# Kernel tuning notes

Measured on AMD Instinct MI355X. Metric: run time of the kernel, lower is better.

## Reference

```python
import jax, jax.numpy as jnp
import numpy as np

B, T, L = 64, 128, 32          # batch, read timesteps, item_len (write phase)
D, R = 256, 1024               # output_dim (= input dim per step), controller rnn_size
N, M = 512, 128                # memory_rows, memory_columns
RH, WH = 1, 1                  # read / write heads
EPS = 1e-8
SCALE = 0.02


def setup_inputs() -> dict:
    key = jax.random.key(0)
    ks = jax.random.split(key, 6)
    in_dim = D + RH * M                      # controller sees [x_t, prev reads]
    head_dim = RH * (M + 6) + WH * (3 * M + 6)  # k,beta,g,s(3),gamma (+erase,add for write)
    return {
        "inputs": jax.random.normal(ks[0], (B, T, D), jnp.float32),
        "W_lstm": jax.random.normal(ks[1], (in_dim, 4 * R), jnp.float32) * SCALE,
        "U_lstm": jax.random.normal(ks[2], (R, 4 * R), jnp.float32) * SCALE,
        "b_lstm": jnp.zeros((4 * R,), jnp.float32),
        "W_heads": jax.random.normal(ks[3], (R, head_dim), jnp.float32) * SCALE,
        "b_heads": jnp.zeros((head_dim,), jnp.float32),
        "W_out": jax.random.normal(ks[4], (R + RH * M, D), jnp.float32) * SCALE,
        "b_out": jnp.zeros((D,), jnp.float32),
    }


def _address(Mem, Mem_norm, k, beta, g, s, gamma, w_prev):
    """NTM content + location addressing. Mem:[B,N,M], returns w:[B,N]."""
    k = jnp.tanh(k)                                   # [B,M]
    beta = jax.nn.softplus(beta)                      # [B,1]
    g = jax.nn.sigmoid(g)                             # [B,1]
    s = jax.nn.softmax(s, axis=-1)                    # [B,3] shifts (-1,0,1)
    gamma = 1.0 + jax.nn.softplus(gamma)              # [B,1]
    # cosine similarity content addressing
    sim = jnp.einsum('bnm,bm->bn', Mem, k) / (
        Mem_norm * jnp.linalg.norm(k, axis=-1, keepdims=True) + EPS)
    w_c = jax.nn.softmax(beta * sim, axis=-1)
    # interpolate with previous weighting
    w_g = g * w_c + (1.0 - g) * w_prev
    # circular convolutional shift over {-1,0,1}
    w_s = (s[:, 0:1] * jnp.roll(w_g, -1, axis=-1)
           + s[:, 1:2] * w_g
           + s[:, 2:3] * jnp.roll(w_g, 1, axis=-1))
    # sharpen
    w_pow = (w_s + EPS) ** gamma
    return w_pow / jnp.sum(w_pow, axis=-1, keepdims=True)


def _run(inputs, W_lstm, U_lstm, b_lstm, W_heads, b_heads, W_out, b_out):
    def step(carry, x_t):
        h, c, reads, w_r, w_w, Mem = carry
        # LSTM controller
        z = jnp.concatenate([x_t, reads], -1) @ W_lstm + h @ U_lstm + b_lstm
        zi, zf, zg, zo = jnp.split(z, 4, axis=-1)
        c = jax.nn.sigmoid(zf) * c + jax.nn.sigmoid(zi) * jnp.tanh(zg)
        h = jax.nn.sigmoid(zo) * jnp.tanh(c)
        # head parameters
        p = h @ W_heads + b_heads
        Mem_norm = jnp.linalg.norm(Mem, axis=-1)  # [B,N]
        new_w_r, new_reads = [], []
        for hh in range(RH):
            o = hh * (M + 6)
            w = _address(Mem, Mem_norm, p[:, o:o + M], p[:, o + M:o + M + 1],
                         p[:, o + M + 1:o + M + 2], p[:, o + M + 2:o + M + 5],
                         p[:, o + M + 5:o + M + 6], w_r[:, hh])
            new_w_r.append(w)
            new_reads.append(jnp.einsum('bn,bnm->bm', w, Mem))
        base, wsz = RH * (M + 6), 3 * M + 6
        new_w_w = []
        for hh in range(WH):
            o = base + hh * wsz
            w = _address(Mem, Mem_norm, p[:, o:o + M], p[:, o + M:o + M + 1],
                         p[:, o + M + 1:o + M + 2], p[:, o + M + 2:o + M + 5],
                         p[:, o + M + 5:o + M + 6], w_w[:, hh])
            erase = jax.nn.sigmoid(p[:, o + M + 6:o + 2 * M + 6])
            add = jnp.tanh(p[:, o + 2 * M + 6:o + 3 * M + 6])
            Mem = Mem * (1.0 - w[:, :, None] * erase[:, None, :]) + w[:, :, None] * add[:, None, :]
            new_w_w.append(w)
        reads = jnp.concatenate(new_reads, -1)
        out = jnp.concatenate([h, reads], -1) @ W_out + b_out
        carry = (h, c, reads, jnp.stack(new_w_r, 1), jnp.stack(new_w_w, 1), Mem)
        return carry, out

    init = (jnp.zeros((B, R)), jnp.zeros((B, R)), jnp.zeros((B, RH * M)),
            jnp.full((B, RH, N), 1.0 / N), jnp.full((B, WH, N), 1.0 / N),
            jnp.full((B, N, M), 1e-6))
    # read phase (inputs) followed by write phase (zero response sheet)
    xs = jnp.concatenate([inputs, jnp.zeros((B, L, D), inputs.dtype)], axis=1)
    xs = jnp.moveaxis(xs, 0, 1)  # [T+L, B, D]
    _, outs = jax.lax.scan(step, init, xs)
    write_outputs = jax.nn.sigmoid(jnp.moveaxis(outs[T:], 0, 1))  # [B, L, D]
    return write_outputs


def reference(inputs, W_lstm, U_lstm, b_lstm, W_heads, b_heads, W_out, b_out):
    return _run(inputs, W_lstm, U_lstm, b_lstm, W_heads, b_heads, W_out, b_out)
```

## Files before the change

kernel.cpp:

```cpp
#include <hip/hip_runtime.h>
#include <hip/hip_fp16.h>
#include <math.h>

#define B 64
#define T_READ 128
#define L_WRITE 32
#define TT 160
#define D 256
#define R 1024
#define N 512
#define M 128
#define HD 524
#define K5K 1152
#define EPS 1e-8f
#define BNM ((size_t)B*N*M)

__device__ __forceinline__ float sigmoidf(float x){ return 1.0f/(1.0f+expf(-x)); }
__device__ __forceinline__ float softplusf(float x){ return (x > 20.f) ? x : log1pf(expf(x)); }

__global__ __launch_bounds__(256) void kx_transpose(const float* __restrict__ x, float* __restrict__ xT){
    __shared__ float tile[64][65];
    const int t = blockIdx.x >> 2, k0 = (blockIdx.x & 3)*64;
    #pragma unroll
    for (int rep = 0; rep < 16; ++rep){
        int idx = rep*256 + threadIdx.x;
        int bl = idx >> 6, kl = idx & 63;
        tile[bl][kl] = x[((size_t)bl*T_READ + t)*D + k0 + kl];
    }
    __syncthreads();
    #pragma unroll
    for (int rep = 0; rep < 16; ++rep){
        int idx = rep*256 + threadIdx.x;
        int kl = idx >> 6, bl = idx & 63;
        xT[((size_t)t*D + k0 + kl)*64 + bl] = tile[bl][kl];
    }
}

__global__ __launch_bounds__(256) void kpack_w(const float* __restrict__ Wl, const float* __restrict__ Ul,
                                               __half* __restrict__ Wreh){
    const int k = blockIdx.x;
    const float* src = (k < 384) ? (Wl + (size_t)k*4096) : (Ul + (size_t)(k-384)*4096);
    #pragma unroll
    for (int it = 0; it < 16; ++it){
        int j = it*256 + threadIdx.x;
        int bk = j >> 4, r = j & 15, q = r >> 2, i = r & 3;
        Wreh[((size_t)bk*1408 + k)*16 + r] = __float2half_rn(src[q*1024 + bk*4 + i]);
    }
}

__global__ __launch_bounds__(256) void kpack_wh(const float* __restrict__ Wh, __half* __restrict__ Whh){
    const int k = blockIdx.x;
    for (int j = threadIdx.x; j < HD; j += 256)
        Whh[(size_t)k*HD + j] = __float2half_rn(Wh[(size_t)k*HD + j]);
}

__global__ void k_init(float* ht, float* c_t, float* rp, float* wst, __half* Mem){
    size_t idx = (size_t)blockIdx.x*blockDim.x + threadIdx.x;
    size_t stride = (size_t)gridDim.x*blockDim.x;
    const __half mi = __float2half(1e-6f);
    for (size_t i = idx; i < BNM; i += stride) Mem[i] = mi;
    for (size_t i = idx; i < R*64; i += stride){ ht[i]=0.f; c_t[i]=0.f; }
    for (size_t i = idx; i < 8*128*64; i += stride) rp[i] = 0.f;
    for (size_t i = idx; i < 4*B*N; i += stride) wst[i] = 1.f/512.f;
}

__global__ __launch_bounds__(1024) void k1_z(
    const float* __restrict__ xT, const __half* __restrict__ Wreh, const float* __restrict__ bl,
    float* __restrict__ ht, float* __restrict__ c_t, const float* __restrict__ rp,
    float* __restrict__ hist, int t)
{
    __shared__ float smem[8192 + 16384];
    const int bk = blockIdx.x;
    const int tid = threadIdx.x, lane = tid & 63, w = tid >> 6;

    for (int e = tid; e < 8192; e += 1024){
        float s = 0.f;
        #pragma unroll
        for (int p = 0; p < 8; ++p) s += rp[p*8192 + e];
        smem[e] = s;
        if (t > T_READ && (e >> 10) == bk)
            hist[((size_t)(t-1-T_READ)*K5K + 1024 + (e>>6))*64 + (e&63)] = s;
    }
    __syncthreads();

    const int r0 = bk*4;
    const int rd = (t < T_READ);
    const int kn = rd ? 88 : 72;
    const int k0 = rd ? w*88 : 256 + w*72;
    const __half* wbase = Wreh + ((size_t)bk*1408 + k0)*16;
    float acc[16];
    #pragma unroll
    for (int i = 0; i < 16; ++i) acc[i] = 0.f;
    #pragma unroll 4
    for (int kk = 0; kk < kn; ++kk){
        int k = k0 + kk;
        float a;
        if (k < 256)      a = xT[((size_t)t*256 + k)*64 + lane];
        else if (k < 384) a = smem[(k-256)*64 + lane];
        else              a = ht[(size_t)(k-384)*64 + lane];
        float4 raw0 = *reinterpret_cast<const float4*>(wbase + (size_t)kk*16);
        float4 raw1 = *reinterpret_cast<const float4*>(wbase + (size_t)kk*16 + 8);
        const __half2* h0 = reinterpret_cast<const __half2*>(&raw0);
        const __half2* h1 = reinterpret_cast<const __half2*>(&raw1);
        float2 f;
        f = __half22float2(h0[0]); acc[0] += a*f.x; acc[1] += a*f.y;
        f = __half22float2(h0[1]); acc[2] += a*f.x; acc[3] += a*f.y;
        f = __half22float2(h0[2]); acc[4] += a*f.x; acc[5] += a*f.y;
        f = __half22float2(h0[3]); acc[6] += a*f.x; acc[7] += a*f.y;
        f = __half22float2(h1[0]); acc[8] += a*f.x; acc[9] += a*f.y;
        f = __half22float2(h1[1]); acc[10]+= a*f.x; acc[11]+= a*f.y;
        f = __half22float2(h1[2]); acc[12]+= a*f.x; acc[13]+= a*f.y;
        f = __half22float2(h1[3]); acc[14]+= a*f.x; acc[15]+= a*f.y;
    }
    float* comb = smem + 8192;
    #pragma unroll
    for (int j = 0; j < 16; ++j) comb[(w*16 + j)*64 + lane] = acc[j];
    __syncthreads();
    if (tid < 256){
        int i = tid >> 6, b2 = tid & 63;
        float g4[4];
        #pragma unroll
        for (int q = 0; q < 4; ++q){
            float s = bl[q*1024 + r0 + i];
            #pragma unroll
            for (int ks = 0; ks < 16; ++ks) s += comb[(ks*16 + q*4 + i)*64 + b2];
            g4[q] = s;
        }
        int ri = (r0 + i)*64 + b2;
        float cn = sigmoidf(g4[1])*c_t[ri] + sigmoidf(g4[0])*tanhf(g4[2]);
        float hn = sigmoidf(g4[3])*tanhf(cn);
        c_t[ri] = cn;
        ht[ri] = hn;
        if (t >= T_READ) hist[((size_t)(t-T_READ)*K5K + r0 + i)*64 + b2] = hn;
    }
}

__global__ __launch_bounds__(512) void k2f(
    const float* __restrict__ ht, const __half* __restrict__ Whh, const float* __restrict__ bh,
    float* __restrict__ khat, float* __restrict__ scal, float* __restrict__ eal)
{
    __shared__ float part[8][2][64];
    const int tid = threadIdx.x, lane = tid & 63, w = tid >> 6;
    const int col0 = blockIdx.x*2;
    const int k0 = w*128;
    float a0 = 0.f, a1 = 0.f;
    #pragma unroll 4
    for (int k = k0; k < k0+128; ++k){
        float a = ht[(size_t)k*64 + lane];
        __half2 wv = *reinterpret_cast<const __half2*>(Whh + (size_t)k*HD + col0);
        float2 f = __half22float2(wv);
        a0 += a*f.x; a1 += a*f.y;
    }
    part[w][0][lane] = a0;
    part[w][1][lane] = a1;
    __syncthreads();
    if (tid < 128){
        int c = tid >> 6, b = tid & 63;
        int col = col0 + c;
        float v = bh[col];
        #pragma unroll
        for (int w2 = 0; w2 < 8; ++w2) v += part[w2][c][b];
        if (col < 128)       khat[b*256 + col] = tanhf(v);
        else if (col < 134){ int i = col-128; scal[b*16 + i]     = (i==0)?softplusf(v):(i==1)?sigmoidf(v):(i==5)?1.f+softplusf(v):v; }
        else if (col < 262)  khat[b*256 + 128 + (col-134)] = tanhf(v);
        else if (col < 268){ int i = col-262; scal[b*16 + 8 + i] = (i==0)?softplusf(v):(i==1)?sigmoidf(v):(i==5)?1.f+softplusf(v):v; }
        else if (col < 396)  eal[b*256 + (col-268)]        = sigmoidf(v);
        else                 eal[b*256 + 128 + (col-396)]  = tanhf(v);
    }
}

__global__ __launch_bounds__(512) void k3_dots(
    const float* __restrict__ khat, const __half* __restrict__ Mem,
    float* __restrict__ mnorm, float* __restrict__ dots)
{
    __shared__ float kh[256];
    const int b = blockIdx.x >> 3, nq = blockIdx.x & 7;
    const int tid = threadIdx.x, lane = tid & 63, w = tid >> 6;
    if (tid < 256) kh[tid] = khat[b*256 + tid];
    __syncthreads();
    float2 kr  = reinterpret_cast<const float2*>(kh)[lane];
    float2 kw2 = reinterpret_cast<const float2*>(kh + 128)[lane];
    #pragma unroll 2
    for (int i = 0; i < 8; ++i){
        int n = nq*64 + w*8 + i;
        const __half* mrow = Mem + ((size_t)b*N + n)*M;
        __half2 mh = *reinterpret_cast<const __half2*>(mrow + lane*2);
        float2 mv = __half22float2(mh);
        float s2 = mv.x*mv.x + mv.y*mv.y;
        float dr = mv.x*kr.x + mv.y*kr.y;
        float dw = mv.x*kw2.x + mv.y*kw2.y;
        #pragma unroll
        for (int off = 32; off; off >>= 1){
            s2 += __shfl_xor(s2, off);
            dr += __shfl_xor(dr, off);
            dw += __shfl_xor(dw, off);
        }
        if (lane == 0){
            mnorm[b*N + n] = sqrtf(s2);
            dots[(b*2+0)*N + n] = dr;
            dots[(b*2+1)*N + n] = dw;
        }
    }
}

__device__ __forceinline__ float blk_sum8g(float v, volatile float* red8, int lane, int wgi){
    #pragma unroll
    for (int off = 32; off; off >>= 1) v += __shfl_xor(v, off);
    if (lane == 0) red8[wgi] = v;
    __syncthreads();
    float r = red8[0]+red8[1]+red8[2]+red8[3]+red8[4]+red8[5]+red8[6]+red8[7];
    __syncthreads();
    return r;
}
__device__ __forceinline__ float blk_max8g(float v, volatile float* red8, int lane, int wgi){
    #pragma unroll
    for (int off = 32; off; off >>= 1) v = fmaxf(v, __shfl_xor(v, off));
    if (lane == 0) red8[wgi] = v;
    __syncthreads();
    float r = fmaxf(fmaxf(fmaxf(red8[0],red8[1]),fmaxf(red8[2],red8[3])),
                    fmaxf(fmaxf(red8[4],red8[5]),fmaxf(red8[6],red8[7])));
    __syncthreads();
    return r;
}

__global__ __launch_bounds__(1024) void k4_addr(
    const float* __restrict__ khat, const float* __restrict__ scal, const float* __restrict__ ealg,
    const float* __restrict__ mnorm, const float* __restrict__ dots,
    float* __restrict__ wst, __half* __restrict__ Mem, float* __restrict__ rp, int t)
{
    __shared__ float kh[256];
    __shared__ float sc[16];
    __shared__ float eal[256];
    __shared__ float wfin[1024];
    __shared__ float wgbuf[1024];
    __shared__ float red8[2][8];
    __shared__ float racc_s[1024];
    const int b = blockIdx.x >> 3, nq = blockIdx.x & 7;
    const int tid = threadIdx.x, lane = tid & 63;

    if (tid < 256)      kh[tid]      = khat[b*256 + tid];
    else if (tid < 272) sc[tid-256]  = scal[b*16 + (tid-256)];
    else if (tid < 528) eal[tid-272] = ealg[b*256 + (tid-272)];
    __syncthreads();

    {
        const int g = tid >> 9;
        const int n = tid & 511;
        const int wgi = (tid >> 6) & 7;
        float* wgl = wgbuf + g*512;
        volatile float* r8 = red8[g];

        float kv = (n < 128) ? kh[g*128 + n] : 0.f;
        float knm = sqrtf(blk_sum8g(kv*kv, r8, lane, wgi));
        float beta = sc[g*8+0], gg = sc[g*8+1], gamma = sc[g*8+5];
        float s0r = sc[g*8+2], s1r = sc[g*8+3], s2r = sc[g*8+4];
        float smx = fmaxf(s0r, fmaxf(s1r, s2r));
        float e0 = expf(s0r-smx), e1 = expf(s1r-smx), e2 = expf(s2r-smx);
        float esum = e0+e1+e2;
        float s0 = e0/esum, s1 = e1/esum, s2 = e2/esum;

        float sim = dots[(b*2+g)*N + n] / (mnorm[b*N + n]*knm + EPS);
        float aa = beta * sim;
        float amax = blk_max8g(aa, r8, lane, wgi);
        float ev = expf(aa - amax);
        float wc = ev / blk_sum8g(ev, r8, lane, wgi);

        const float* wpr = wst + ((size_t)((t&1)*2 + g))*(B*N);
        float*       wnx = wst + ((size_t)(((t+1)&1)*2 + g))*(B*N);
        float wprev = wpr[b*N + n];
        float wgv = gg*wc + (1.f - gg)*wprev;
        wgl[n] = wgv; __syncthreads();
        float wsv = s0*wgl[(n+1)&511] + s1*wgv + s2*wgl[(n-1)&511];
        float wp2 = powf(wsv + EPS, gamma);
        float wsum = blk_sum8g(wp2, r8, lane, wgi);
        float wv = wp2 / wsum;
        wfin[g*512 + n] = wv;
        if (nq == 0) wnx[b*N + n] = wv;
        __syncthreads();
    }

    {
        const int m = tid & 127, ns = tid >> 7;
        const float e  = eal[m];
        const float ad = eal[128 + m];
        float racc = 0.f;
        #pragma unroll 4
        for (int i2 = 0; i2 < 8; ++i2){
            int nn = nq*64 + i2*8 + ns;
            size_t idx = ((size_t)b*N + nn)*M + m;
            float v = __half2float(Mem[idx]);
            float wr = wfin[nn], ww = wfin[512 + nn];
            racc += wr*v;
            Mem[idx] = __float2half_rn(v*(1.f - ww*e) + ww*ad);
        }
        racc_s[tid] = racc;
        __syncthreads();
        if (tid < 128){
            float s = 0.f;
            #pragma unroll
            for (int g2 = 0; g2 < 8; ++g2) s += racc_s[g2*128 + tid];
            rp[(size_t)nq*8192 + tid*64 + b] = s;
        }
    }
}

__global__ __launch_bounds__(256) void k_fin(const float* __restrict__ rp, float* __restrict__ hist){
    int e = blockIdx.x*256 + threadIdx.x;
    float s = 0.f;
    #pragma unroll
    for (int p = 0; p < 8; ++p) s += rp[p*8192 + e];
    hist[((size_t)31*K5K + 1024 + (e>>6))*64 + (e&63)] = s;
}

__global__ __launch_bounds__(512) void k5_out(
    const float* __restrict__ hist, const float* __restrict__ Wo, const float* __restrict__ bo,
    float* __restrict__ out)
{
    __shared__ float smem[16384];
    const int tid = threadIdx.x, lane = tid & 63, w = tid >> 6;
    const int l = blockIdx.x >> 3, jg = blockIdx.x & 7;
    const int j0 = jg*32;
    float acc[32];
    #pragma unroll
    for (int i = 0; i < 32; ++i) acc[i] = 0.f;
    const int k0 = w*144;
    #pragma unroll 2
    for (int kk = 0; kk < 144; ++kk){
        int k = k0 + kk;
        float a = hist[((size_t)l*K5K + k)*64 + lane];
        const float* wrow = Wo + (size_t)k*D + j0;
        #pragma unroll
        for (int qq = 0; qq < 8; ++qq){
            float4 wv = *reinterpret_cast<const float4*>(wrow + qq*4);
            acc[qq*4+0] += a*wv.x; acc[qq*4+1] += a*wv.y;
            acc[qq*4+2] += a*wv.z; acc[qq*4+3] += a*wv.w;
        }
    }
    __syncthreads();
    #pragma unroll
    for (int c = 0; c < 32; ++c) smem[(w*32 + c)*64 + lane] = acc[c];
    __syncthreads();
    {
        const int b2 = tid >> 3, jq = tid & 7;
        float4 ov;
        float* po = (float*)&ov;
        #pragma unroll
        for (int i = 0; i < 4; ++i){
            int c = jq*4 + i;
            float s = bo[j0 + c];
            #pragma unroll
            for (int ks = 0; ks < 8; ++ks) s += smem[(ks*32 + c)*64 + b2];
            po[i] = sigmoidf(s);
        }
        *reinterpret_cast<float4*>(out + ((size_t)b2*L_WRITE + l)*D + j0 + jq*4) = ov;
    }
}

extern "C" void kernel_launch(void* const* d_in, const int* in_sizes, int n_in,
                              void* d_out, int out_size, void* d_ws, size_t ws_size,
                              hipStream_t stream)
{
    const float* x   = (const float*)d_in[0];
    const float* Wl  = (const float*)d_in[1];
    const float* Ul  = (const float*)d_in[2];
    const float* bl  = (const float*)d_in[3];
    const float* Wh  = (const float*)d_in[4];
    const float* bh  = (const float*)d_in[5];
    const float* Wo  = (const float*)d_in[6];
    const float* bo  = (const float*)d_in[7];
    float* out = (float*)d_out;

    float* ws = (float*)d_ws;
    float* xT    = ws; ws += (size_t)T_READ*D*64;
    __half* Wreh = (__half*)ws; ws += (size_t)1408*4096/2;
    __half* Whh  = (__half*)ws; ws += (size_t)1024*HD/2 + 64;
    float* ht    = ws; ws += (size_t)R*64;
    float* c_t   = ws; ws += (size_t)R*64;
    float* khat  = ws; ws += (size_t)B*256;
    float* scal  = ws; ws += (size_t)B*16;
    float* eal   = ws; ws += (size_t)B*256;
    float* mnorm = ws; ws += (size_t)B*N;
    float* dots  = ws; ws += (size_t)B*2*N;
    float* wst   = ws; ws += (size_t)4*B*N;
    __half* Mem  = (__half*)ws; ws += BNM/2;
    float* rp    = ws; ws += (size_t)8*128*64;
    float* hist  = ws; ws += (size_t)L_WRITE*K5K*64;

    hipLaunchKernelGGL(kx_transpose, dim3(T_READ*4), dim3(256), 0, stream, x, xT);
    hipLaunchKernelGGL(kpack_w,      dim3(1408),     dim3(256), 0, stream, Wl, Ul, Wreh);
    hipLaunchKernelGGL(kpack_wh,     dim3(1024),     dim3(256), 0, stream, Wh, Whh);
    hipLaunchKernelGGL(k_init,       dim3(2048),     dim3(256), 0, stream, ht, c_t, rp, wst, Mem);

    for (int t = 0; t < TT; ++t){
        hipLaunchKernelGGL(k1_z,    dim3(256), dim3(1024), 0, stream, xT, Wreh, bl, ht, c_t, rp, hist, t);
        hipLaunchKernelGGL(k2f,     dim3(262), dim3(512),  0, stream, ht, Whh, bh, khat, scal, eal);
        hipLaunchKernelGGL(k3_dots, dim3(512), dim3(512),  0, stream, khat, Mem, mnorm, dots);
        hipLaunchKernelGGL(k4_addr, dim3(512), dim3(1024), 0, stream, khat, scal, eal, mnorm, dots, wst, Mem, rp, t);
    }
    hipLaunchKernelGGL(k_fin,  dim3(32),  dim3(256), 0, stream, rp, hist);
    hipLaunchKernelGGL(k5_out, dim3(256), dim3(512), 0, stream, hist, Wo, bo, out);
}
```

Measured before the change: 11.28 ms.

## Replace partial-read buffer reduction with double-buffered atomic accumulation

Per-step read vectors were stored as 8 partial slices, and every k1_z block summed all of them into shared memory. Now k4_addr atomically adds its partials into one of two ping-pong buffers, which k3_dots of the next step zeroes, so k1_z reads the finished vector straight from global memory. This removes the redundant 8-way reduction that all 256 blocks repeated, at the cost of atomic traffic and non-deterministic summation order. Separately, k2f now uses 1024 threads with a 64-row K split per wave instead of 128, to add parallelism to the head projection.

```diff
diff --git a/kernel.cpp b/kernel.cpp
--- a/kernel.cpp
+++ b/kernel.cpp
@@ -54,34 +54,30 @@
         Whh[(size_t)k*HD + j] = __float2half_rn(Wh[(size_t)k*HD + j]);
 }
 
-__global__ void k_init(float* ht, float* c_t, float* rp, float* wst, __half* Mem){
+__global__ void k_init(float* ht, float* c_t, float* reads_fin, float* wst, __half* Mem){
     size_t idx = (size_t)blockIdx.x*blockDim.x + threadIdx.x;
     size_t stride = (size_t)gridDim.x*blockDim.x;
     const __half mi = __float2half(1e-6f);
     for (size_t i = idx; i < BNM; i += stride) Mem[i] = mi;
     for (size_t i = idx; i < R*64; i += stride){ ht[i]=0.f; c_t[i]=0.f; }
-    for (size_t i = idx; i < 8*128*64; i += stride) rp[i] = 0.f;
+    for (size_t i = idx; i < 2*128*64; i += stride) reads_fin[i] = 0.f;
     for (size_t i = idx; i < 4*B*N; i += stride) wst[i] = 1.f/512.f;
 }
 
 __global__ __launch_bounds__(1024) void k1_z(
     const float* __restrict__ xT, const __half* __restrict__ Wreh, const float* __restrict__ bl,
-    float* __restrict__ ht, float* __restrict__ c_t, const float* __restrict__ rp,
+    float* __restrict__ ht, float* __restrict__ c_t, const float* __restrict__ reads_fin,
     float* __restrict__ hist, int t)
 {
-    __shared__ float smem[8192 + 16384];
+    __shared__ float comb[16384];
     const int bk = blockIdx.x;
     const int tid = threadIdx.x, lane = tid & 63, w = tid >> 6;
-
-    for (int e = tid; e < 8192; e += 1024){
-        float s = 0.f;
-        #pragma unroll
-        for (int p = 0; p < 8; ++p) s += rp[p*8192 + e];
-        smem[e] = s;
-        if (t > T_READ && (e >> 10) == bk)
-            hist[((size_t)(t-1-T_READ)*K5K + 1024 + (e>>6))*64 + (e&63)] = s;
-    }
-    __syncthreads();
+    const float* rf = reads_fin + (size_t)(t & 1)*8192;
+
+    if (t > T_READ && bk < 8){
+        int e = bk*1024 + tid;
+        hist[((size_t)(t-1-T_READ)*K5K + 1024 + (e>>6))*64 + (e&63)] = rf[e];
+    }
 
     const int r0 = bk*4;
     const int rd = (t < T_READ);
@@ -96,7 +92,7 @@
         int k = k0 + kk;
         float a;
         if (k < 256)      a = xT[((size_t)t*256 + k)*64 + lane];
-        else if (k < 384) a = smem[(k-256)*64 + lane];
+        else if (k < 384) a = rf[(k-256)*64 + lane];
         else              a = ht[(size_t)(k-384)*64 + lane];
         float4 raw0 = *reinterpret_cast<const float4*>(wbase + (size_t)kk*16);
         float4 raw1 = *reinterpret_cast<const float4*>(wbase + (size_t)kk*16 + 8);
@@ -112,7 +108,6 @@
         f = __half22float2(h1[2]); acc[12]+= a*f.x; acc[13]+= a*f.y;
         f = __half22float2(h1[3]); acc[14]+= a*f.x; acc[15]+= a*f.y;
     }
-    float* comb = smem + 8192;
     #pragma unroll
     for (int j = 0; j < 16; ++j) comb[(w*16 + j)*64 + lane] = acc[j];
     __syncthreads();
@@ -135,17 +130,17 @@
     }
 }
 
-__global__ __launch_bounds__(512) void k2f(
+__global__ __launch_bounds__(1024) void k2f(
     const float* __restrict__ ht, const __half* __restrict__ Whh, const float* __restrict__ bh,
     float* __restrict__ khat, float* __restrict__ scal, float* __restrict__ eal)
 {
-    __shared__ float part[8][2][64];
+    __shared__ float part[16][2][64];
     const int tid = threadIdx.x, lane = tid & 63, w = tid >> 6;
     const int col0 = blockIdx.x*2;
-    const int k0 = w*128;
+    const int k0 = w*64;
     float a0 = 0.f, a1 = 0.f;
     #pragma unroll 4
-    for (int k = k0; k < k0+128; ++k){
+    for (int k = k0; k < k0+64; ++k){
         float a = ht[(size_t)k*64 + lane];
         __half2 wv = *reinterpret_cast<const __half2*>(Whh + (size_t)k*HD + col0);
         float2 f = __half22float2(wv);
@@ -159,7 +154,7 @@
         int col = col0 + c;
         float v = bh[col];
         #pragma unroll
-        for (int w2 = 0; w2 < 8; ++w2) v += part[w2][c][b];
+        for (int w2 = 0; w2 < 16; ++w2) v += part[w2][c][b];
         if (col < 128)       khat[b*256 + col] = tanhf(v);
         else if (col < 134){ int i = col-128; scal[b*16 + i]     = (i==0)?softplusf(v):(i==1)?sigmoidf(v):(i==5)?1.f+softplusf(v):v; }
         else if (col < 262)  khat[b*256 + 128 + (col-134)] = tanhf(v);
@@ -171,11 +166,16 @@
 
 __global__ __launch_bounds__(512) void k3_dots(
     const float* __restrict__ khat, const __half* __restrict__ Mem,
-    float* __restrict__ mnorm, float* __restrict__ dots)
+    float* __restrict__ mnorm, float* __restrict__ dots, float* __restrict__ reads_fin, int t)
 {
     __shared__ float kh[256];
     const int b = blockIdx.x >> 3, nq = blockIdx.x & 7;
     const int tid = threadIdx.x, lane = tid & 63, w = tid >> 6;
+    if (blockIdx.x < 8){
+        int e = blockIdx.x*1024 + tid;
+        reads_fin[(size_t)(t & 1)*8192 + e] = 0.f;
+        reads_fin[(size_t)(t & 1)*8192 + e + 512] = 0.f;
+    }
     if (tid < 256) kh[tid] = khat[b*256 + tid];
     __syncthreads();
     float2 kr  = reinterpret_cast<const float2*>(kh)[lane];
@@ -226,7 +226,7 @@
 __global__ __launch_bounds__(1024) void k4_addr(
     const float* __restrict__ khat, const float* __restrict__ scal, const float* __restrict__ ealg,
     const float* __restrict__ mnorm, const float* __restrict__ dots,
-    float* __restrict__ wst, __half* __restrict__ Mem, float* __restrict__ rp, int t)
+    float* __restrict__ wst, __half* __restrict__ Mem, float* __restrict__ reads_fin, int t)
 {
     __shared__ float kh[256];
     __shared__ float sc[16];
@@ -299,16 +299,14 @@
             float s = 0.f;
             #pragma unroll
             for (int g2 = 0; g2 < 8; ++g2) s += racc_s[g2*128 + tid];
-            rp[(size_t)nq*8192 + tid*64 + b] = s;
-        }
-    }
-}
-
-__global__ __launch_bounds__(256) void k_fin(const float* __restrict__ rp, float* __restrict__ hist){
+            atomicAdd(&reads_fin[(size_t)((t+1) & 1)*8192 + tid*64 + b], s);
+        }
+    }
+}
+
+__global__ __launch_bounds__(256) void k_fin(const float* __restrict__ reads_fin, float* __restrict__ hist){
     int e = blockIdx.x*256 + threadIdx.x;
-    float s = 0.f;
-    #pragma unroll
-    for (int p = 0; p < 8; ++p) s += rp[p*8192 + e];
+    float s = reads_fin[(size_t)(TT & 1)*8192 + e];
     hist[((size_t)31*K5K + 1024 + (e>>6))*64 + (e&63)] = s;
 }
 
@@ -383,20 +381,20 @@
     float* dots  = ws; ws += (size_t)B*2*N;
     float* wst   = ws; ws += (size_t)4*B*N;
     __half* Mem  = (__half*)ws; ws += BNM/2;
-    float* rp    = ws; ws += (size_t)8*128*64;
+    float* reads_fin = ws; ws += (size_t)2*128*64;
     float* hist  = ws; ws += (size_t)L_WRITE*K5K*64;
 
     hipLaunchKernelGGL(kx_transpose, dim3(T_READ*4), dim3(256), 0, stream, x, xT);
     hipLaunchKernelGGL(kpack_w,      dim3(1408),     dim3(256), 0, stream, Wl, Ul, Wreh);
     hipLaunchKernelGGL(kpack_wh,     dim3(1024),     dim3(256), 0, stream, Wh, Whh);
-    hipLaunchKernelGGL(k_init,       dim3(2048),     dim3(256), 0, stream, ht, c_t, rp, wst, Mem);
+    hipLaunchKernelGGL(k_init,       dim3(2048),     dim3(256), 0, stream, ht, c_t, reads_fin, wst, Mem);
 
     for (int t = 0; t < TT; ++t){
-        hipLaunchKernelGGL(k1_z,    dim3(256), dim3(1024), 0, stream, xT, Wreh, bl, ht, c_t, rp, hist, t);
-        hipLaunchKernelGGL(k2f,     dim3(262), dim3(512),  0, stream, ht, Whh, bh, khat, scal, eal);
-        hipLaunchKernelGGL(k3_dots, dim3(512), dim3(512),  0, stream, khat, Mem, mnorm, dots);
-        hipLaunchKernelGGL(k4_addr, dim3(512), dim3(1024), 0, stream, khat, scal, eal, mnorm, dots, wst, Mem, rp, t);
-    }
-    hipLaunchKernelGGL(k_fin,  dim3(32),  dim3(256), 0, stream, rp, hist);
+        hipLaunchKernelGGL(k1_z,    dim3(256), dim3(1024), 0, stream, xT, Wreh, bl, ht, c_t, reads_fin, hist, t);
+        hipLaunchKernelGGL(k2f,     dim3(262), dim3(1024), 0, stream, ht, Whh, bh, khat, scal, eal);
+        hipLaunchKernelGGL(k3_dots, dim3(512), dim3(512),  0, stream, khat, Mem, mnorm, dots, reads_fin, t);
+        hipLaunchKernelGGL(k4_addr, dim3(512), dim3(1024), 0, stream, khat, scal, eal, mnorm, dots, wst, Mem, reads_fin, t);
+    }
+    hipLaunchKernelGGL(k_fin,  dim3(32),  dim3(256), 0, stream, reads_fin, hist);
     hipLaunchKernelGGL(k5_out, dim3(256), dim3(512), 0, stream, hist, Wo, bo, out);
 }
```

Result: faster. 10.63 ms (median of 2 runs) (-5.7%).
